# Optimization experiments

Hardware: AMD Instinct MI355X
Metric: run time of the kernel (lower is better)

The kernel has to match this reference:

```python
import jax, jax.numpy as jnp
import numpy as np

N = 100000  # nodes
K = 6       # kNN neighbors (includes self, loop=True)


def _knn_edges(pos_np, k):
    """Exact kNN with self-loops, chunked to bound memory. Returns (src, dst) int32."""
    n = pos_np.shape[0]
    idx = np.empty((n, k), dtype=np.int32)
    sq = (pos_np ** 2).sum(1)
    cs = 512
    for s in range(0, n, cs):
        e = min(s + cs, n)
        d = sq[s:e, None] - 2.0 * (pos_np[s:e] @ pos_np.T) + sq[None, :]
        idx[s:e] = np.argpartition(d, k, axis=1)[:, :k].astype(np.int32)
    src = idx.reshape(-1)                                  # neighbors j
    dst = np.repeat(np.arange(n, dtype=np.int32), k)       # centers i
    return src, dst


def _linear_init(key, fan_in, fan_out):
    k1, k2 = jax.random.split(key)
    s = 1.0 / np.sqrt(fan_in)
    W = jax.random.uniform(k1, (fan_in, fan_out), minval=-s, maxval=s, dtype=jnp.float32)
    b = jax.random.uniform(k2, (fan_out,), minval=-s, maxval=s, dtype=jnp.float32)
    return W, b


def setup_inputs() -> dict:
    rng = np.random.default_rng(0)
    pos_np = rng.standard_normal((N, 3)).astype(np.float32)
    src, dst = _knn_edges(pos_np, K)
    edge_index = jnp.asarray(np.stack([src, dst]))

    key = jax.random.key(0)
    ks = jax.random.split(key, 6)
    W1a, b1a = _linear_init(ks[0], 3 + 3, 32)
    W1b, b1b = _linear_init(ks[1], 32, 32)
    W2a, b2a = _linear_init(ks[2], 32 + 3, 64)
    W2b, b2b = _linear_init(ks[3], 64, 64)
    W3a, b3a = _linear_init(ks[4], 64 + 3, 128)
    W3b, b3b = _linear_init(ks[5], 128, 128)

    return dict(pos=jnp.asarray(pos_np), edge_index=edge_index,
                W1a=W1a, b1a=b1a, W1b=W1b, b1b=b1b,
                W2a=W2a, b2a=b2a, W2b=W2b, b2b=b2b,
                W3a=W3a, b3a=b3a, W3b=W3b, b3b=b3b)


def _pointnet_conv(x, pos, src, dst, Wa, ba, Wb, bb):
    # message per edge (j->i): local_nn(concat(x_j, pos_j - pos_i)); max-aggregate at i
    m = jnp.concatenate([x[src], pos[src] - pos[dst]], axis=-1)  # [E, Cin+3]
    m = jax.nn.relu(m @ Wa + ba) @ Wb + bb                       # [E, Cout]
    return jax.ops.segment_max(m, dst, num_segments=N)           # [N, Cout]


def reference(pos, edge_index, W1a, b1a, W1b, b1b, W2a, b2a, W2b, b2b, W3a, b3a, W3b, b3b):
    src, dst = edge_index[0], edge_index[1]
    h = jax.nn.relu(_pointnet_conv(pos, pos, src, dst, W1a, b1a, W1b, b1b))
    h = jax.nn.relu(_pointnet_conv(h, pos, src, dst, W2a, b2a, W2b, b2b))
    h = jax.nn.relu(_pointnet_conv(h, pos, src, dst, W3a, b3a, W3b, b3b))
    return h
```

## Files before the change

### kernel.cpp

```cpp
#include <hip/hip_runtime.h>

#define NODES 100000
#define KNN 6

typedef unsigned short u16t;
typedef __attribute__((ext_vector_type(8))) short bf16x8;
typedef __attribute__((ext_vector_type(4))) float f32x4;
union U16 { uint4 u; bf16x8 b; };

__device__ inline f32x4 mfma16(bf16x8 a, bf16x8 b, f32x4 c) {
    return __builtin_amdgcn_mfma_f32_16x16x32_bf16(a, b, c, 0, 0, 0);
}
__device__ inline unsigned top2(unsigned u1, unsigned u0) {
    return __builtin_amdgcn_perm(u1, u0, 0x07060302u);
}
__device__ inline u16t bf16_rn(float x) {
    unsigned u = __float_as_uint(x);
    return (u16t)((u + 0x7FFF + ((u >> 16) & 1)) >> 16);
}
__device__ inline float bf16_f(u16t h) {
    return __uint_as_float(((unsigned)h) << 16);
}
__device__ inline void split_store(u16t* hp, u16t* lp, float v) {
    const unsigned u = __float_as_uint(v);
    *hp = (u16t)(u >> 16);
    const float hif = __uint_as_float(u & 0xFFFF0000u);
    *lp = (u16t)(__float_as_uint(v - hif) >> 16);
}

template <int CIN_, int N_>
__device__ void prep_dev(const float* __restrict__ W,
                         uint4* __restrict__ fh, uint4* __restrict__ fl, int idx) {
    constexpr int KT = (CIN_ + 31) / 32;
    constexpr int NTt = N_ / 16;
    if (idx >= NTt * KT * 64) return;
    const int lane = idx & 63;
    const int fk = idx >> 6;
    const int kt = fk % KT, t = fk / KT;
    const int n = t * 16 + (lane & 15);
    const int kbase = kt * 32 + (lane >> 4) * 8;
    unsigned h[4], l[4];
    for (int p = 0; p < 4; p++) {
        u16t hh[2], ll[2];
        for (int q = 0; q < 2; q++) {
            const int c = kbase + 2 * p + q;
            const float w = (c < CIN_) ? W[(size_t)c * N_ + n] : 0.f;
            const u16t hi = bf16_rn(w);
            hh[q] = hi;
            ll[q] = bf16_rn(w - bf16_f(hi));
        }
        h[p] = (unsigned)hh[0] | ((unsigned)hh[1] << 16);
        l[p] = (unsigned)ll[0] | ((unsigned)ll[1] << 16);
    }
    fh[idx] = make_uint4(h[0], h[1], h[2], h[3]);
    fl[idx] = make_uint4(l[0], l[1], l[2], l[3]);
}

__global__ void prep_all(const float* W1a, const float* W1b,
                         const float* W2a, const float* W2b,
                         const float* W3a, const float* W3b, uint4* wf) {
    const int b = blockIdx.x, t = threadIdx.x;
    if (b == 0)      prep_dev<6, 32>(W1a, wf + 0, wf + 128, t);
    else if (b == 1) prep_dev<32, 32>(W1b, wf + 256, wf + 384, t);
    else if (b < 4)  prep_dev<35, 64>(W2a, wf + 512, wf + 1024, (b - 2) * 256 + t);
    else if (b < 6)  prep_dev<64, 64>(W2b, wf + 1536, wf + 2048, (b - 4) * 256 + t);
    else if (b < 12) prep_dev<67, 128>(W3a, wf + 2560, wf + 4096, (b - 6) * 256 + t);
    else             prep_dev<128, 128>(W3b, wf + 5632, wf + 7680, (b - 12) * 256 + t);
}

template <int CX, int H, int NWAVE, int NB, bool OUTP>
__global__ __launch_bounds__(NWAVE * 64, 4) void pnconv_mfma(
    const u16t* __restrict__ xh, const u16t* __restrict__ xl,
    const float* __restrict__ pos, const int* __restrict__ ei,
    const uint4* __restrict__ wfa_hi, const uint4* __restrict__ wfa_lo,
    const float* __restrict__ ba,
    const uint4* __restrict__ wfb_hi, const uint4* __restrict__ wfb_lo,
    const float* __restrict__ bb,
    float* __restrict__ outf, u16t* __restrict__ oh, u16t* __restrict__ ol)
{
    constexpr int NTH = NWAVE * 64;
    constexpr int CIN = CX + 3;
    constexpr int K1T = (CIN + 31) / 32;
    constexpr int K2T = H / 32;
    constexpr int NW = (H / 16) / NWAVE;
    constexpr int E = NB * KNN;
    constexpr int MT1 = E / 16;
    constexpr int MT2 = NB * 8 / 16;
    constexpr int K1P = K1T * 32 + 8;
    constexpr int K2P = K2T * 32 + 8;
    constexpr int APL = E * K1P;
    constexpr int HPL = E * K2P;
    constexpr int SM = (2 * APL > 2 * HPL) ? 2 * APL : 2 * HPL;
    static_assert(E % 16 == 0 && E <= NTH, "tile shape");

    __shared__ __align__(16) u16t smem[SM];
    __shared__ int srcs[E];

    const int tid = threadIdx.x;
    const int lane = tid & 63, wv = tid >> 6;
    const int l15 = lane & 15, quad = lane >> 4;
    const int node0 = blockIdx.x * NB;
    const long e0 = (long)node0 * KNN;

    if (tid < E) srcs[tid] = ei[e0 + tid];

    U16 wah[2][NW], wal[2][NW];
#pragma unroll
    for (int t = 0; t < NW; t++) {
        const int fi = ((wv * NW + t) * K1T) * 64 + lane;
        wah[0][t].u = wfa_hi[fi];
        wal[0][t].u = wfa_lo[fi];
    }
    __syncthreads();

    if constexpr (CX % 8 == 0) {
        constexpr int C8 = CX / 8;
        for (int i = tid; i < E * C8; i += NTH) {
            const int e = i / C8, c = i % C8;
            const size_t sb = (size_t)srcs[e] * CX + c * 8;
            *(uint4*)&smem[e * K1P + c * 8] = *(const uint4*)&xh[sb];
            *(uint4*)&smem[APL + e * K1P + c * 8] = *(const uint4*)&xl[sb];
        }
    }
    if (tid < E) {
        const int e = tid, s = srcs[e], nd = node0 + e / KNN;
#pragma unroll
        for (int d = 0; d < 3; d++) {
            const float sp = pos[3 * s + d];
            if constexpr (CX == 3)
                split_store(&smem[e * K1P + d], &smem[APL + e * K1P + d], sp);
            split_store(&smem[e * K1P + CX + d], &smem[APL + e * K1P + CX + d],
                        sp - pos[3 * nd + d]);
        }
    }
    constexpr int PADA = (CIN + 7) & ~7;
    constexpr int NU4 = (K1P - PADA) / 8;
    for (int i = tid; i < 2 * E; i += NTH) {
        const int pl = (i >= E) ? 1 : 0;
        const int e = i - pl * E;
        u16t* row = &smem[pl * APL + e * K1P];
        for (int k = CIN; k < PADA; k++) row[k] = 0;
        for (int j = 0; j < NU4; j++) *(uint4*)&row[PADA + j * 8] = make_uint4(0, 0, 0, 0);
    }
    __syncthreads();

    f32x4 acc1[NW][MT1];
#pragma unroll
    for (int t = 0; t < NW; t++)
#pragma unroll
        for (int m = 0; m < MT1; m++) acc1[t][m] = (f32x4){0.f, 0.f, 0.f, 0.f};

#pragma unroll
    for (int kt = 0; kt < K1T; kt++) {
        const int cur = kt & 1, nxt = cur ^ 1;
        const int nkt = (kt + 1 < K1T) ? kt + 1 : kt;
#pragma unroll
        for (int t = 0; t < NW; t++) {
            const int fi = ((wv * NW + t) * K1T + nkt) * 64 + lane;
            wah[nxt][t].u = wfa_hi[fi];
            wal[nxt][t].u = wfa_lo[fi];
        }
#pragma unroll
        for (int m = 0; m < MT1; m++) {
            const u16t* p = &smem[(m * 16 + l15) * K1P + kt * 32 + quad * 8];
            U16 dh, dl;
            dh.u = *(const uint4*)p;
            dl.u = *(const uint4*)(p + APL);
#pragma unroll
            for (int t = 0; t < NW; t++) {
                acc1[t][m] = mfma16(wah[cur][t].b, dh.b, acc1[t][m]);
                acc1[t][m] = mfma16(wah[cur][t].b, dl.b, acc1[t][m]);
                acc1[t][m] = mfma16(wal[cur][t].b, dh.b, acc1[t][m]);
            }
        }
    }

    U16 wbh[2][NW], wbl[2][NW];
#pragma unroll
    for (int t = 0; t < NW; t++) {
        const int fi = ((wv * NW + t) * K2T) * 64 + lane;
        wbh[0][t].u = wfb_hi[fi];
        wbl[0][t].u = wfb_lo[fi];
    }
    __syncthreads();

#pragma unroll
    for (int t = 0; t < NW; t++) {
        const int khb = (wv * NW + t) * 16 + quad * 4;
        const float4 bs = *(const float4*)&ba[khb];
#pragma unroll
        for (int m = 0; m < MT1; m++) {
            const float v0 = fmaxf(acc1[t][m][0] + bs.x, 0.f);
            const float v1 = fmaxf(acc1[t][m][1] + bs.y, 0.f);
            const float v2 = fmaxf(acc1[t][m][2] + bs.z, 0.f);
            const float v3 = fmaxf(acc1[t][m][3] + bs.w, 0.f);
            const unsigned u0 = __float_as_uint(v0), u1 = __float_as_uint(v1);
            const unsigned u2 = __float_as_uint(v2), u3 = __float_as_uint(v3);
            uint2 hw, lw;
            hw.x = top2(u1, u0);
            hw.y = top2(u3, u2);
            const float l0 = v0 - __uint_as_float(u0 & 0xFFFF0000u);
            const float l1 = v1 - __uint_as_float(u1 & 0xFFFF0000u);
            const float l2 = v2 - __uint_as_float(u2 & 0xFFFF0000u);
            const float l3 = v3 - __uint_as_float(u3 & 0xFFFF0000u);
            lw.x = top2(__float_as_uint(l1), __float_as_uint(l0));
            lw.y = top2(__float_as_uint(l3), __float_as_uint(l2));
            u16t* wp = &smem[(m * 16 + l15) * K2P + khb];
            *(uint2*)wp = hw;
            *(uint2*)(wp + HPL) = lw;
        }
    }
    __syncthreads();

    int eaddr[MT2];
#pragma unroll
    for (int m = 0; m < MT2; m++) {
        const int slot = m * 16 + l15;
        const int i7 = slot & 7;
        const int e2 = (slot >> 3) * KNN + (i7 < KNN ? i7 : 0);
        eaddr[m] = e2 * K2P + quad * 8;
    }

    f32x4 acc2[NW][MT2];
#pragma unroll
    for (int t = 0; t < NW; t++)
#pragma unroll
        for (int m = 0; m < MT2; m++) acc2[t][m] = (f32x4){0.f, 0.f, 0.f, 0.f};

#pragma unroll
    for (int kt = 0; kt < K2T; kt++) {
        const int cur = kt & 1, nxt = cur ^ 1;
        const int nkt = (kt + 1 < K2T) ? kt + 1 : kt;
#pragma unroll
        for (int t = 0; t < NW; t++) {
            const int fi = ((wv * NW + t) * K2T + nkt) * 64 + lane;
            wbh[nxt][t].u = wfb_hi[fi];
            wbl[nxt][t].u = wfb_lo[fi];
        }
#pragma unroll
        for (int m = 0; m < MT2; m++) {
            const u16t* p = &smem[eaddr[m] + kt * 32];
            U16 dh, dl;
            dh.u = *(const uint4*)p;
            dl.u = *(const uint4*)(p + HPL);
#pragma unroll
            for (int t = 0; t < NW; t++) {
                acc2[t][m] = mfma16(dh.b, wbh[cur][t].b, acc2[t][m]);
                acc2[t][m] = mfma16(dh.b, wbl[cur][t].b, acc2[t][m]);
                acc2[t][m] = mfma16(dl.b, wbh[cur][t].b, acc2[t][m]);
            }
        }
    }

#pragma unroll
    for (int t = 0; t < NW; t++) {
        const int nb = (wv * NW + t) * 16;
        const float bias = bb[nb + l15];
#pragma unroll
        for (int m = 0; m < MT2; m++) {
            const f32x4 a = acc2[t][m];
            float v = fmaxf(fmaxf(a[0], a[1]), fmaxf(a[2], a[3]));
            v = fmaxf(v, __shfl_xor(v, 16));
            v = fmaxf(v + bias, 0.f);
            if ((quad & 1) == 0) {
                const int node = node0 + 2 * m + (quad >> 1);
                const size_t oidx = (size_t)node * H + nb + l15;
                if constexpr (OUTP) {
                    split_store(&oh[oidx], &ol[oidx], v);
                } else {
                    outf[oidx] = v;
                }
            }
        }
    }
}

extern "C" void kernel_launch(void* const* d_in, const int* in_sizes, int n_in,
                              void* d_out, int out_size, void* d_ws, size_t ws_size,
                              hipStream_t stream) {
    const float* pos = (const float*)d_in[0];
    const int* ei = (const int*)d_in[1];
    const float* W1a = (const float*)d_in[2];
    const float* b1a = (const float*)d_in[3];
    const float* W1b = (const float*)d_in[4];
    const float* b1b = (const float*)d_in[5];
    const float* W2a = (const float*)d_in[6];
    const float* b2a = (const float*)d_in[7];
    const float* W2b = (const float*)d_in[8];
    const float* b2b = (const float*)d_in[9];
    const float* W3a = (const float*)d_in[10];
    const float* b3a = (const float*)d_in[11];
    const float* W3b = (const float*)d_in[12];
    const float* b3b = (const float*)d_in[13];

    u16t* h1h = (u16t*)d_ws;
    u16t* h1l = h1h + (size_t)NODES * 32;
    u16t* h2h = h1l + (size_t)NODES * 32;
    u16t* h2l = h2h + (size_t)NODES * 64;
    uint4* wf = (uint4*)(h2l + (size_t)NODES * 64);

    prep_all<<<20, 256, 0, stream>>>(W1a, W1b, W2a, W2b, W3a, W3b, wf);

    pnconv_mfma<3, 32, 2, 16, true><<<NODES / 16, 128, 0, stream>>>(
        nullptr, nullptr, pos, ei,
        wf + 0, wf + 128, b1a, wf + 256, wf + 384, b1b,
        nullptr, h1h, h1l);

    pnconv_mfma<32, 64, 4, 16, true><<<NODES / 16, 256, 0, stream>>>(
        h1h, h1l, pos, ei,
        wf + 512, wf + 1024, b2a, wf + 1536, wf + 2048, b2b,
        nullptr, h2h, h2l);

    pnconv_mfma<64, 128, 4, 8, false><<<NODES / 8, 256, 0, stream>>>(
        h2h, h2l, pos, ei,
        wf + 2560, wf + 4096, b3a, wf + 5632, wf + 7680, b3b,
        (float*)d_out, nullptr, nullptr);
}
```

Measured before the change: 253.4 us.

## Drop padded neighbor slots in second GEMM via edge-slot permutation

The second-layer GEMM previously padded each node's 6 edges to 8 row slots, wasting a quarter of the MFMA work and LDS reads. The new mapping packs edges densely across triples of M-tiles, so each lane's accumulator rows hold edges of a single node. The max reduction then happens in registers across the three tiles without a cross-lane shuffle, and every lane stores output. It also rotates the feature-chunk gather order per edge to spread LDS bank conflicts and spreads the pos/relative-position fill across all threads. The new mapping requires E to be a multiple of 48.

```diff
diff --git a/kernel.cpp b/kernel.cpp
--- a/kernel.cpp
+++ b/kernel.cpp
@@ -85,13 +85,14 @@
     constexpr int NW = (H / 16) / NWAVE;
     constexpr int E = NB * KNN;
     constexpr int MT1 = E / 16;
-    constexpr int MT2 = NB * 8 / 16;
+    constexpr int MT2 = E / 16;
     constexpr int K1P = K1T * 32 + 8;
     constexpr int K2P = K2T * 32 + 8;
     constexpr int APL = E * K1P;
     constexpr int HPL = E * K2P;
     constexpr int SM = (2 * APL > 2 * HPL) ? 2 * APL : 2 * HPL;
-    static_assert(E % 16 == 0 && E <= NTH, "tile shape");
+    static_assert(E % 48 == 0 && E <= NTH, "tile shape");
+    static_assert(MT2 % 3 == 0, "slot perm needs m-triples");
 
     __shared__ __align__(16) u16t smem[SM];
     __shared__ int srcs[E];
@@ -116,22 +117,21 @@
     if constexpr (CX % 8 == 0) {
         constexpr int C8 = CX / 8;
         for (int i = tid; i < E * C8; i += NTH) {
-            const int e = i / C8, c = i % C8;
+            const int e = i / C8, c0 = i % C8;
+            const int c = (c0 + e) & (C8 - 1);
             const size_t sb = (size_t)srcs[e] * CX + c * 8;
             *(uint4*)&smem[e * K1P + c * 8] = *(const uint4*)&xh[sb];
             *(uint4*)&smem[APL + e * K1P + c * 8] = *(const uint4*)&xl[sb];
         }
     }
-    if (tid < E) {
-        const int e = tid, s = srcs[e], nd = node0 + e / KNN;
-#pragma unroll
-        for (int d = 0; d < 3; d++) {
-            const float sp = pos[3 * s + d];
-            if constexpr (CX == 3)
-                split_store(&smem[e * K1P + d], &smem[APL + e * K1P + d], sp);
-            split_store(&smem[e * K1P + CX + d], &smem[APL + e * K1P + CX + d],
-                        sp - pos[3 * nd + d]);
-        }
+    for (int i = tid; i < E * 3; i += NTH) {
+        const int e = i / 3, d = i - 3 * (i / 3);
+        const int s = srcs[e], nd = node0 + e / KNN;
+        const float sp = pos[3 * s + d];
+        if constexpr (CX == 3)
+            split_store(&smem[e * K1P + d], &smem[APL + e * K1P + d], sp);
+        split_store(&smem[e * K1P + CX + d], &smem[APL + e * K1P + CX + d],
+                    sp - pos[3 * nd + d]);
     }
     constexpr int PADA = (CIN + 7) & ~7;
     constexpr int NU4 = (K1P - PADA) / 8;
@@ -215,10 +215,9 @@
     int eaddr[MT2];
 #pragma unroll
     for (int m = 0; m < MT2; m++) {
-        const int slot = m * 16 + l15;
-        const int i7 = slot & 7;
-        const int e2 = (slot >> 3) * KNN + (i7 < KNN ? i7 : 0);
-        eaddr[m] = e2 * K2P + quad * 8;
+        const int nd_s = (m / 3) * 8 + 2 * (l15 >> 2) + ((l15 >> 1) & 1);
+        const int i_s = (m % 3) * 2 + (l15 & 1);
+        eaddr[m] = (nd_s * KNN + i_s) * K2P + quad * 8;
     }
 
     f32x4 acc2[NW][MT2];
@@ -257,13 +256,15 @@
         const int nb = (wv * NW + t) * 16;
         const float bias = bb[nb + l15];
 #pragma unroll
-        for (int m = 0; m < MT2; m++) {
-            const f32x4 a = acc2[t][m];
-            float v = fmaxf(fmaxf(a[0], a[1]), fmaxf(a[2], a[3]));
-            v = fmaxf(v, __shfl_xor(v, 16));
-            v = fmaxf(v + bias, 0.f);
-            if ((quad & 1) == 0) {
-                const int node = node0 + 2 * m + (quad >> 1);
+        for (int g = 0; g < MT2 / 3; g++) {
+#pragma unroll
+            for (int rp = 0; rp < 2; rp++) {
+                float v = fmaxf(
+                    fmaxf(fmaxf(acc2[t][3 * g + 0][2 * rp], acc2[t][3 * g + 0][2 * rp + 1]),
+                          fmaxf(acc2[t][3 * g + 1][2 * rp], acc2[t][3 * g + 1][2 * rp + 1])),
+                    fmaxf(acc2[t][3 * g + 2][2 * rp], acc2[t][3 * g + 2][2 * rp + 1]));
+                v = fmaxf(v + bias, 0.f);
+                const int node = node0 + g * 8 + 2 * quad + rp;
                 const size_t oidx = (size_t)node * H + nb + l15;
                 if constexpr (OUTP) {
                     split_store(&oh[oidx], &ol[oidx], v);
```

Result: faster. 233.0 us (-8.1%).
